# Performance work log

Measured on AMD Instinct MI355X. Metric: run time of the kernel, lower is better.

## Reference

```python
import jax, jax.numpy as jnp
import numpy as np

NUM_GROUPS = 32
EPS = 1e-5


def group_norm(x, w, b):
    # x: [B,C,H,W], 32 groups
    B, C, H, W = x.shape
    xg = x.reshape(B, NUM_GROUPS, C // NUM_GROUPS, H, W)
    mean = xg.mean(axis=(2, 3, 4), keepdims=True)
    var = xg.var(axis=(2, 3, 4), keepdims=True)
    xn = ((xg - mean) * jax.lax.rsqrt(var + EPS)).reshape(B, C, H, W)
    return xn * w[None, :, None, None] + b[None, :, None, None]


def conv1x1(x, w, b):
    # x: [B,C,H,W], w: [O,C], b: [O]
    return jnp.einsum('bchw,oc->bohw', x, w) + b[None, :, None, None]


def setup_inputs() -> dict:
    key = jax.random.key(0)
    ks = jax.random.split(key, 7)
    B, C, H, W = 16, 512, 32, 32
    x = jax.random.normal(ks[0], (B, C, H, W), dtype=jnp.float32)
    gn_w = jnp.ones((C,), dtype=jnp.float32)
    gn_b = jnp.zeros((C,), dtype=jnp.float32)
    s = 1.0 / np.sqrt(C)
    qkv_w = jax.random.normal(ks[1], (3 * C, C), dtype=jnp.float32) * s
    qkv_b = jnp.zeros((3 * C,), dtype=jnp.float32)
    proj_w = jax.random.normal(ks[2], (C, C), dtype=jnp.float32) * s
    proj_b = jnp.zeros((C,), dtype=jnp.float32)
    return {"x": x, "gn_w": gn_w, "gn_b": gn_b, "qkv_w": qkv_w,
            "qkv_b": qkv_b, "proj_w": proj_w, "proj_b": proj_b}


def reference(x, gn_w, gn_b, qkv_w, qkv_b, proj_w, proj_b):
    B, C, H, W = x.shape
    qkv = conv1x1(group_norm(x, gn_w, gn_b), qkv_w, qkv_b)
    q, k, v = jnp.split(qkv, 3, axis=1)
    scale = (C // 8) ** (-0.5)
    # attn: [B, h, w, H, W]
    attn = jnp.einsum('bchw,bcHW->bhwHW', q * scale, k)
    # NOTE: faithful to original torch code: softmax over the LAST axis only
    attn = jax.nn.softmax(attn, axis=-1)
    out = jnp.einsum('bhwHW,bcHW->bchw', attn, v)
    return x + conv1x1(out, proj_w, proj_b)
```

## Files before the change

kernel.cpp:

```cpp
#include <hip/hip_runtime.h>
#include <hip/hip_bf16.h>

#define B_    16
#define C_    512
#define S_    1024
#define NGRP  32
#define CPG   16

typedef __attribute__((ext_vector_type(8))) short  short8;
typedef __attribute__((ext_vector_type(4))) short  short4v;
typedef __attribute__((ext_vector_type(4))) float  floatx4;

__device__ __forceinline__ unsigned short f2bf(float f) {
    __hip_bfloat16 h = __float2bfloat16(f);
    unsigned short u;
    __builtin_memcpy(&u, &h, 2);
    return u;
}

__global__ __launch_bounds__(256)
void gn_fused_kernel(const float* __restrict__ x, const float* __restrict__ w,
                     const float* __restrict__ bias, __hip_bfloat16* __restrict__ xnT) {
    int bg = blockIdx.x;
    int b = bg >> 5, g = bg & 31;
    const float4* xp = (const float4*)(x + (size_t)bg * (CPG * S_));
    int tid = threadIdx.x;

    float4 vv[16];
    float s = 0.f, ss = 0.f;
#pragma unroll
    for (int r = 0; r < 16; ++r) {
        float4 v = xp[r * 256 + tid];
        vv[r] = v;
        s  += v.x + v.y + v.z + v.w;
        ss += v.x*v.x + v.y*v.y + v.z*v.z + v.w*v.w;
    }
    for (int off = 32; off > 0; off >>= 1) {
        s  += __shfl_down(s, off);
        ss += __shfl_down(ss, off);
    }
    __shared__ float red[2][4];
    __shared__ float msh[2];
    int wid = tid >> 6, lane = tid & 63;
    if (lane == 0) { red[0][wid] = s; red[1][wid] = ss; }
    __syncthreads();
    if (tid == 0) {
        float a = 0.f, c = 0.f;
        for (int i = 0; i < 4; ++i) { a += red[0][i]; c += red[1][i]; }
        float mean = a / (float)(CPG * S_);
        float var  = c / (float)(CPG * S_) - mean * mean;
        msh[0] = mean;
        msh[1] = rsqrtf(var + 1e-5f);
    }
    __syncthreads();
    float mean = msh[0], inv = msh[1];

    float sc[16], sh[16];
#pragma unroll
    for (int c = 0; c < 16; ++c) {
        float wc = w[g * 16 + c];
        sc[c] = inv * wc;
        sh[c] = bias[g * 16 + c] - mean * inv * wc;
    }

#pragma unroll
    for (int kk = 0; kk < 4; ++kk) {
        unsigned short outp[16];
#pragma unroll
        for (int c = 0; c < 16; ++c) {
            float v = (kk == 0) ? vv[c].x : (kk == 1) ? vv[c].y : (kk == 2) ? vv[c].z : vv[c].w;
            outp[c] = f2bf(v * sc[c] + sh[c]);
        }
        int srow = 4 * tid + kk;
        unsigned short* dst = (unsigned short*)xnT + ((size_t)(b * S_ + srow) * C_ + g * 16);
        *(short8*)dst       = *(short8*)outp;
        *(short8*)(dst + 8) = *(short8*)(outp + 8);
    }
}

__global__ __launch_bounds__(256)
void prep_kernel(const float* __restrict__ qkv_w, const float* __restrict__ proj_w,
                 const float* __restrict__ qkv_b,
                 unsigned short* __restrict__ bufX,
                 unsigned short* __restrict__ bufY,
                 float* __restrict__ bqWk, float* __restrict__ biasvp)
{
    int blk = blockIdx.x;
    int tid = threadIdx.x;
    if (blk < 192) {
        __shared__ float T[64][65];
        int mat = blk >> 6, tile = blk & 63;
        int r0 = (tile >> 3) * 64, c0 = (tile & 7) * 64;
        const float* src; unsigned short* dst;
        if (mat == 0)      { src = qkv_w + 512 * 512;  dst = bufX; }
        else if (mat == 1) { src = qkv_w;              dst = bufY; }
        else               { src = qkv_w + 1024 * 512; dst = bufY + 262144; }
#pragma unroll
        for (int rr = 0; rr < 4; ++rr) {
            int sr = rr * 16 + (tid >> 4);
            int sc = (tid & 15) * 4;
            float4 v = *(const float4*)(src + (size_t)(c0 + sr) * 512 + r0 + sc);
            T[sc][sr] = v.x; T[sc + 1][sr] = v.y; T[sc + 2][sr] = v.z; T[sc + 3][sr] = v.w;
        }
        __syncthreads();
#pragma unroll
        for (int rr = 0; rr < 4; ++rr) {
            int dr = rr * 16 + (tid >> 4);
            int dc = (tid & 15) * 4;
            short4v o;
            o[0] = (short)f2bf(T[dr][dc]);     o[1] = (short)f2bf(T[dr][dc + 1]);
            o[2] = (short)f2bf(T[dr][dc + 2]); o[3] = (short)f2bf(T[dr][dc + 3]);
            *(short4v*)(dst + (size_t)(r0 + dr) * 512 + c0 + dc) = o;
        }
    } else if (blk < 256) {
        unsigned short* wp = bufX + 262144;
#pragma unroll
        for (int t = 0; t < 4; ++t) {
            int i = (blk - 192) * 4096 + t * 1024 + tid * 4;
            float4 v = *(const float4*)(proj_w + i);
            short4v o;
            o[0] = (short)f2bf(v.x); o[1] = (short)f2bf(v.y);
            o[2] = (short)f2bf(v.z); o[3] = (short)f2bf(v.w);
            *(short4v*)(wp + i) = o;
        }
    } else if (blk < 264) {
        int sub = blk - 256;
        int j = (sub & 1) * 256 + tid;
        int o0 = (sub >> 1) * 128;
        float acc = 0.f;
#pragma unroll 8
        for (int oo = 0; oo < 128; ++oo) {
            int o = o0 + oo;
            acc += qkv_b[o] * qkv_w[(size_t)(512 + o) * 512 + j];
        }
        atomicAdd(&bqWk[j], acc);
    } else {
        int wv = tid >> 6, lane = tid & 63;
        int c = (blk - 264) * 4 + wv;
        float s = 0.f;
#pragma unroll
        for (int t = 0; t < 8; ++t)
            s += proj_w[(size_t)c * 512 + t * 64 + lane] * qkv_b[1024 + t * 64 + lane];
        for (int off = 32; off > 0; off >>= 1) s += __shfl_down(s, off);
        if (lane == 0) biasvp[c] = s;
    }
}

template<int BIAS_MODE, bool OUT_BF16, bool RESID, bool SWIZ, int KTOT>
__global__ __launch_bounds__(256)
void mfma_gemm(const unsigned short* __restrict__ A, const unsigned short* __restrict__ Bm,
               const float* __restrict__ bias, const float* __restrict__ resid,
               void* __restrict__ Yv,
               int lda, int ldb, int ldy,
               size_t sA, size_t sB, size_t sY, size_t sR, float alpha,
               int ntsh, int nxsh)
{
    __shared__ unsigned short As[2 * 128 * 32];
    __shared__ unsigned short Bs[2 * 128 * 32];
    int bx, by, bz;
    if (SWIZ) {
        int lin = blockIdx.x;
        int xcd = lin & 7, sup = lin >> 3;
        bz = xcd + ((sup >> ntsh) << 3);
        int tile = sup & ((1 << ntsh) - 1);
        bx = tile & ((1 << nxsh) - 1);
        by = tile >> nxsh;
    } else { bx = blockIdx.x; by = blockIdx.y; bz = blockIdx.z; }

    const unsigned short* Ab = A  + (size_t)bz * sA;
    const unsigned short* Bb = Bm + (size_t)bz * sB;
    const int tid = threadIdx.x, wave = tid >> 6, lane = tid & 63;
    const int m0 = by * 128, n0 = bx * 128;
    const int wr = wave >> 1, wc = wave & 1, lr = lane & 15, kq = lane >> 4;
    const int row0 = tid >> 2, kc0 = (tid & 3) << 3;

    floatx4 acc[4][4] = {};

    for (int k0 = 0; k0 < KTOT; k0 += 64) {
        __syncthreads();
#pragma unroll
        for (int kk = 0; kk < 2; ++kk) {
#pragma unroll
            for (int r = 0; r < 2; ++r) {
                const unsigned short* ga = Ab + (size_t)(m0 + r * 64 + row0) * lda + k0 + kk * 32 + kc0;
                __builtin_amdgcn_global_load_lds(
                    (const __attribute__((address_space(1))) void*)ga,
                    (__attribute__((address_space(3))) void*)(As + kk * 4096 + (r * 256 + wave * 64) * 8),
                    16, 0, 0);
                const unsigned short* gb = Bb + (size_t)(n0 + r * 64 + row0) * ldb + k0 + kk * 32 + kc0;
                __builtin_amdgcn_global_load_lds(
                    (const __attribute__((address_space(1))) void*)gb,
                    (__attribute__((address_space(3))) void*)(Bs + kk * 4096 + (r * 256 + wave * 64) * 8),
                    16, 0, 0);
            }
        }
        __syncthreads();

#pragma unroll
        for (int kk = 0; kk < 2; ++kk) {
            short8 af[4], bfr[4];
#pragma unroll
            for (int i = 0; i < 4; ++i)
                af[i] = *(const short8*)&As[kk * 4096 + (wr * 64 + i * 16 + lr) * 32 + kq * 8];
#pragma unroll
            for (int j = 0; j < 4; ++j)
                bfr[j] = *(const short8*)&Bs[kk * 4096 + (wc * 64 + j * 16 + lr) * 32 + kq * 8];
#pragma unroll
            for (int i = 0; i < 4; ++i)
#pragma unroll
                for (int j = 0; j < 4; ++j)
                    acc[i][j] = __builtin_amdgcn_mfma_f32_16x16x32_bf16(af[i], bfr[j], acc[i][j], 0, 0, 0);
        }
    }

    const size_t ybase = (size_t)bz * sY;
    const size_t rbase = (size_t)bz * sR;
#pragma unroll
    for (int i = 0; i < 4; ++i) {
#pragma unroll
        for (int r = 0; r < 4; ++r) {
            int m = m0 + wr * 64 + i * 16 + kq * 4 + r;
            float bm = (BIAS_MODE == 1) ? bias[m] : 0.f;
#pragma unroll
            for (int j = 0; j < 4; ++j) {
                int n = n0 + wc * 64 + j * 16 + lr;
                float vv = acc[i][j][r] * alpha + bm;
                if (BIAS_MODE == 2) vv += bias[n];
                if (RESID) vv += resid[rbase + (size_t)m * ldy + n];
                if (OUT_BF16)
                    ((__hip_bfloat16*)Yv)[ybase + (size_t)m * ldy + n] = __float2bfloat16(vv);
                else
                    ((float*)Yv)[ybase + (size_t)m * ldy + n] = vv;
            }
        }
    }
}

__global__ __launch_bounds__(512)
void scores_softmax8(const unsigned short* __restrict__ A,
                     const unsigned short* __restrict__ Bm,
                     unsigned short* __restrict__ P)
{
    __shared__ __align__(16) unsigned short lds[65536];
    char* asb = (char*)lds;
    char* bsb = (char*)lds + 65536;

    const int bid = blockIdx.x;
    const int bz = bid >> 4, t16 = bid & 15;
    const int by = t16 >> 2, bx = t16 & 3;
    const int m0 = by << 8, n0 = bx << 8;

    const size_t sAB = (size_t)S_ * 512;
    const unsigned short* Ab = A  + (size_t)bz * sAB;
    const unsigned short* Bb = Bm + (size_t)bz * sAB;

    const int tid = threadIdx.x, wave = tid >> 6, lane = tid & 63;
    const int wr = wave >> 2, wc = wave & 3;
    const int lr = lane & 15, kq = lane >> 4;
    const int swz = (lr & 7) << 4;

    floatx4 acc[8][4] = {};
    short8 aF[4][2], bF[2][2][2];

    auto stage = [&](const unsigned short* __restrict__ G, int row0, int t,
                     char* base, int buf, int half) {
#pragma unroll
        for (int c = 0; c < 2; ++c) {
            int x = c * 8192 + tid * 16;
            int row = x >> 7;
            int colb = (x & 127) ^ ((row & 7) << 4);
            const unsigned short* ga = G + (((size_t)(row0 + row)) << 9) + (t << 6) + (colb >> 1);
            char* ldst = base + buf * 32768 + half * 16384 + c * 8192 + wave * 1024;
            __builtin_amdgcn_global_load_lds(
                (const __attribute__((address_space(1))) void*)ga,
                (__attribute__((address_space(3))) void*)ldst, 16, 0, 0);
        }
    };
    auto rdA = [&](int buf, int mh, int ii, int kk) {
        int byte = buf * 32768 + wr * 16384 + (mh * 64 + ii * 16 + lr) * 128
                 + ((kk * 64 + kq * 16) ^ swz);
        return *(const short8*)(asb + byte);
    };
    auto rdB = [&](int buf, int nh, int jj, int kk) {
        int trow = wc * 64 + (nh * 2 + jj) * 16 + lr;
        int byte = buf * 32768 + (trow >> 7) * 16384 + (trow & 127) * 128
                 + ((kk * 64 + kq * 16) ^ swz);
        return *(const short8*)(bsb + byte);
    };

    stage(Ab, m0,       0, asb, 0, 0);
    stage(Bb, n0,       0, bsb, 0, 0);
    stage(Bb, n0 + 128, 0, bsb, 0, 1);
    stage(Ab, m0 + 128, 0, asb, 0, 1);
    stage(Ab, m0,       1, asb, 1, 0);
    stage(Bb, n0,       1, bsb, 1, 0);
    stage(Bb, n0 + 128, 1, bsb, 1, 1);
    asm volatile("s_waitcnt vmcnt(6)" ::: "memory");
    __builtin_amdgcn_s_barrier();

    for (int t = 0; t < 8; ++t) {
        const int buf = t & 1;
#pragma unroll
        for (int ii = 0; ii < 4; ++ii) { aF[ii][0] = rdA(buf, 0, ii, 0); aF[ii][1] = rdA(buf, 0, ii, 1); }
#pragma unroll
        for (int jj = 0; jj < 2; ++jj) { bF[0][jj][0] = rdB(buf, 0, jj, 0); bF[0][jj][1] = rdB(buf, 0, jj, 1); }
        if (t < 7) stage(Ab, m0 + 128, t + 1, asb, (t + 1) & 1, 1);
        __builtin_amdgcn_s_barrier();
        asm volatile("s_waitcnt lgkmcnt(0)" ::: "memory");
        __builtin_amdgcn_s_setprio(1);
#pragma unroll
        for (int ii = 0; ii < 4; ++ii)
#pragma unroll
            for (int jj = 0; jj < 2; ++jj)
#pragma unroll
                for (int kk = 0; kk < 2; ++kk)
                    acc[ii][jj] = __builtin_amdgcn_mfma_f32_16x16x32_bf16(aF[ii][kk], bF[0][jj][kk], acc[ii][jj], 0, 0, 0);
        __builtin_amdgcn_s_setprio(0);
        __builtin_amdgcn_s_barrier();
#pragma unroll
        for (int jj = 0; jj < 2; ++jj) { bF[1][jj][0] = rdB(buf, 1, jj, 0); bF[1][jj][1] = rdB(buf, 1, jj, 1); }
        __builtin_amdgcn_s_barrier();
        asm volatile("s_waitcnt lgkmcnt(0)" ::: "memory");
        __builtin_amdgcn_s_setprio(1);
#pragma unroll
        for (int ii = 0; ii < 4; ++ii)
#pragma unroll
            for (int jj = 0; jj < 2; ++jj)
#pragma unroll
                for (int kk = 0; kk < 2; ++kk)
                    acc[ii][2 + jj] = __builtin_amdgcn_mfma_f32_16x16x32_bf16(aF[ii][kk], bF[1][jj][kk], acc[ii][2 + jj], 0, 0, 0);
        __builtin_amdgcn_s_setprio(0);
        __builtin_amdgcn_s_barrier();
#pragma unroll
        for (int ii = 0; ii < 4; ++ii) { aF[ii][0] = rdA(buf, 1, ii, 0); aF[ii][1] = rdA(buf, 1, ii, 1); }
        if (t < 6) stage(Bb, n0, t + 2, bsb, buf, 0);
        __builtin_amdgcn_s_barrier();
        asm volatile("s_waitcnt lgkmcnt(0)" ::: "memory");
        __builtin_amdgcn_s_setprio(1);
#pragma unroll
        for (int ii = 0; ii < 4; ++ii)
#pragma unroll
            for (int jj = 0; jj < 2; ++jj)
#pragma unroll
                for (int kk = 0; kk < 2; ++kk)
                    acc[4 + ii][2 + jj] = __builtin_amdgcn_mfma_f32_16x16x32_bf16(aF[ii][kk], bF[1][jj][kk], acc[4 + ii][2 + jj], 0, 0, 0);
        __builtin_amdgcn_s_setprio(0);
        __builtin_amdgcn_s_barrier();
        if (t < 6) {
            stage(Ab, m0,       t + 2, asb, buf, 0);
            stage(Bb, n0 + 128, t + 2, bsb, buf, 1);
        }
        __builtin_amdgcn_s_setprio(1);
#pragma unroll
        for (int ii = 0; ii < 4; ++ii)
#pragma unroll
            for (int jj = 0; jj < 2; ++jj)
#pragma unroll
                for (int kk = 0; kk < 2; ++kk)
                    acc[4 + ii][jj] = __builtin_amdgcn_mfma_f32_16x16x32_bf16(aF[ii][kk], bF[0][jj][kk], acc[4 + ii][jj], 0, 0, 0);
        __builtin_amdgcn_s_setprio(0);
        if (t < 6) { asm volatile("s_waitcnt vmcnt(6)" ::: "memory"); }
        else       { asm volatile("s_waitcnt vmcnt(0)" ::: "memory"); }
        __builtin_amdgcn_s_barrier();
    }

#pragma unroll
    for (int j = 0; j < 4; ++j) {
        int sqc = wc * 64 + j * 16 + lr;
        int srow = sqc * 512;
        int sxor = (sqc & 7) << 4;
#pragma unroll
        for (int h = 0; h < 4; ++h) {
            float v0[4], v1[4];
            float mx = -1e30f;
#pragma unroll
            for (int r = 0; r < 4; ++r) {
                v0[r] = acc[2 * h][j][r]     * 0.125f;
                v1[r] = acc[2 * h + 1][j][r] * 0.125f;
                mx = fmaxf(mx, fmaxf(v0[r], v1[r]));
            }
            mx = fmaxf(mx, __shfl_xor(mx, 16));
            mx = fmaxf(mx, __shfl_xor(mx, 32));
            float sm = 0.f;
#pragma unroll
            for (int r = 0; r < 4; ++r) {
                v0[r] = __expf(v0[r] - mx);
                v1[r] = __expf(v1[r] - mx);
                sm += v0[r] + v1[r];
            }
            sm += __shfl_xor(sm, 16);
            sm += __shfl_xor(sm, 32);
            float inv = 1.f / sm;
            short4v p0, p1;
#pragma unroll
            for (int r = 0; r < 4; ++r) {
                p0[r] = (short)f2bf(v0[r] * inv);
                p1[r] = (short)f2bf(v1[r] * inv);
            }
            int kb = (wr * 128 + h * 32 + kq * 4) * 2;
            *(short4v*)(asb + ((srow + kb) ^ sxor))      = p0;
            *(short4v*)(asb + ((srow + kb + 32) ^ sxor)) = p1;
        }
    }
    __syncthreads();

    const size_t pbase = ((size_t)bz << 20) + (size_t)n0 * 1024 + m0;
#pragma unroll
    for (int it = 0; it < 16; ++it) {
        int row = wave * 32 + it * 2 + (lane >> 5);
        int colb = (lane & 31) << 4;
        short8 v = *(const short8*)(asb + ((row * 512 + colb) ^ ((row & 7) << 4)));
        *(short8*)(P + pbase + (size_t)row * 1024 + (colb >> 1)) = v;
    }
}

extern "C" void kernel_launch(void* const* d_in, const int* in_sizes, int n_in,
                              void* d_out, int out_size, void* d_ws, size_t ws_size,
                              hipStream_t stream) {
    const float* x     = (const float*)d_in[0];
    const float* gn_w  = (const float*)d_in[1];
    const float* gn_b  = (const float*)d_in[2];
    const float* qkv_w = (const float*)d_in[3];
    const float* qkv_b = (const float*)d_in[4];
    const float* pr_w  = (const float*)d_in[5];
    const float* pr_b  = (const float*)d_in[6];
    float* out = (float*)d_out;

    char* w = (char*)d_ws;
    __hip_bfloat16* xnT  = (__hip_bfloat16*)w;
    __hip_bfloat16* u    = (__hip_bfloat16*)(w + (16u << 20));
    __hip_bfloat16* Vp   = (__hip_bfloat16*)(w + (32u << 20));
    __hip_bfloat16* P    = (__hip_bfloat16*)(w + (48u << 20));
    unsigned short* bufX = (unsigned short*)(w + (80u << 20));
    unsigned short* bufY = (unsigned short*)(w + (81u << 20));
    unsigned short* bufZ = (unsigned short*)(w + (82u << 20));
    float*          bqWk = (float*)(w + (83u << 20));
    float*          bvp  = (float*)(w + (83u << 20) + 4096);

    hipMemsetAsync(bqWk, 0, 512 * sizeof(float), stream);

    prep_kernel<<<392, 256, 0, stream>>>(qkv_w, pr_w, qkv_b, bufX, bufY, bqWk, bvp);

    gn_fused_kernel<<<B_ * NGRP, 256, 0, stream>>>(x, gn_w, gn_b, xnT);

    mfma_gemm<0, true, false, false, 512><<<dim3(4, 4, 2), 256, 0, stream>>>(
        bufX, bufY, nullptr, nullptr, bufZ,
        512, 512, 512, 262144, 262144, 262144, 0, 1.f, 0, 0);

    mfma_gemm<2, true, false, false, 512><<<dim3(4, 128, 1), 256, 0, stream>>>(
        (const unsigned short*)xnT, bufZ, bqWk, nullptr, u,
        512, 512, 512, 0, 0, 0, 0, 1.f, 0, 0);

    mfma_gemm<1, true, false, true, 512><<<512, 256, 0, stream>>>(
        bufZ + 262144, (const unsigned short*)xnT, bvp, nullptr, Vp,
        512, 512, 1024, 0, (size_t)S_ * 512, (size_t)512 * S_, 0, 1.f, 5, 3);

    scores_softmax8<<<256, 512, 0, stream>>>(
        (const unsigned short*)xnT, (const unsigned short*)u, (unsigned short*)P);

    mfma_gemm<1, false, true, true, 1024><<<512, 256, 0, stream>>>(
        (const unsigned short*)Vp, (const unsigned short*)P, pr_b, x, out,
        1024, 1024, 1024, (size_t)512 * S_, (size_t)S_ * S_, (size_t)512 * S_,
        (size_t)512 * S_, 1.f, 5, 3);
}
```

Baseline: 209.6 us.

## Replace three GEMMs with 8-wave 128x256 tile kernel using phased LDS pipeline

Adds a new 512-thread GEMM kernel with 128x256 tiles that loads via global_load_lds into an XOR-swizzled double buffer. The inner loop is split into four MFMA phases, with barriers and s_setprio interleaving the LDS reads and next-tile loads with compute. The Q-proj, V-proj and final output GEMMs switch to it, with grid and swizzle shifts adjusted for the larger tiles. The goal is better latency hiding and data reuse per block. In exchange it uses more LDS per block, lowers occupancy and halves the block count.

```diff
diff --git a/kernel.cpp b/kernel.cpp
--- a/kernel.cpp
+++ b/kernel.cpp
@@ -236,6 +236,161 @@
     }
 }
 
+template<int BIAS_MODE, bool OUT_BF16, bool RESID, bool SWIZ, int KTOT>
+__global__ __launch_bounds__(512)
+void gemm8ph(const unsigned short* __restrict__ A, const unsigned short* __restrict__ Bm,
+             const float* __restrict__ bias, const float* __restrict__ resid,
+             void* __restrict__ Yv,
+             int lda, int ldb, int ldy,
+             size_t sA, size_t sB, size_t sY, size_t sR, float alpha,
+             int ntsh, int nxsh)
+{
+    __shared__ __align__(16) char lds[98304];
+    char* asb = lds;
+    char* bsb = lds + 32768;
+
+    int bx, by, bz;
+    if (SWIZ) {
+        int lin = blockIdx.x;
+        int xcd = lin & 7, sup = lin >> 3;
+        bz = xcd + ((sup >> ntsh) << 3);
+        int tile = sup & ((1 << ntsh) - 1);
+        bx = tile & ((1 << nxsh) - 1);
+        by = tile >> nxsh;
+    } else { bx = blockIdx.x; by = blockIdx.y; bz = blockIdx.z; }
+
+    const unsigned short* Ab = A  + (size_t)bz * sA;
+    const unsigned short* Bb = Bm + (size_t)bz * sB;
+    const int tid = threadIdx.x, wave = tid >> 6, lane = tid & 63;
+    const int m0 = by * 128, n0 = bx * 256;
+    const int wr = wave >> 2, wc = wave & 3;
+    const int lr = lane & 15, kq = lane >> 4;
+    const int swz = (lr & 7) << 4;
+
+    floatx4 acc[4][4] = {};
+    short8 aF[2][2], bF[2][2][2];
+
+    auto stage = [&](const unsigned short* __restrict__ G, int ld, int grow,
+                     int t, char* dstbase) {
+#pragma unroll
+        for (int c = 0; c < 2; ++c) {
+            int x = c * 8192 + tid * 16;
+            int row = x >> 7;
+            int colb = (x & 127) ^ ((row & 7) << 4);
+            const unsigned short* ga = G + (size_t)(grow + row) * ld + t * 64 + (colb >> 1);
+            char* ldst = dstbase + c * 8192 + wave * 1024;
+            __builtin_amdgcn_global_load_lds(
+                (const __attribute__((address_space(1))) void*)ga,
+                (__attribute__((address_space(3))) void*)ldst, 16, 0, 0);
+        }
+    };
+    auto rdA = [&](int buf, int i, int kk) {
+        int byte = buf * 16384 + (wr * 64 + i * 16 + lr) * 128
+                 + ((kk * 64 + kq * 16) ^ swz);
+        return *(const short8*)(asb + byte);
+    };
+    auto rdB = [&](int buf, int jn, int kk) {
+        int row = wc * 64 + jn * 16 + lr;
+        int byte = buf * 32768 + (row >> 7) * 16384 + (row & 127) * 128
+                 + ((kk * 64 + kq * 16) ^ swz);
+        return *(const short8*)(bsb + byte);
+    };
+
+    stage(Ab, lda, m0,       0, asb);
+    stage(Bb, ldb, n0,       0, bsb);
+    stage(Bb, ldb, n0 + 128, 0, bsb + 16384);
+    stage(Bb, ldb, n0,       1, bsb + 32768);
+    stage(Bb, ldb, n0 + 128, 1, bsb + 32768 + 16384);
+    asm volatile("s_waitcnt vmcnt(4)" ::: "memory");
+    __builtin_amdgcn_s_barrier();
+
+    constexpr int NT = KTOT / 64;
+    for (int t = 0; t < NT; ++t) {
+        const int buf = t & 1;
+#pragma unroll
+        for (int ii = 0; ii < 2; ++ii) { aF[ii][0] = rdA(buf, ii, 0); aF[ii][1] = rdA(buf, ii, 1); }
+#pragma unroll
+        for (int jj = 0; jj < 2; ++jj) { bF[0][jj][0] = rdB(buf, jj, 0); bF[0][jj][1] = rdB(buf, jj, 1); }
+        if (t < NT - 1) stage(Ab, lda, m0, t + 1, asb + ((t + 1) & 1) * 16384);
+        __builtin_amdgcn_s_barrier();
+        asm volatile("s_waitcnt lgkmcnt(0)" ::: "memory");
+        __builtin_amdgcn_s_setprio(1);
+#pragma unroll
+        for (int ii = 0; ii < 2; ++ii)
+#pragma unroll
+            for (int jj = 0; jj < 2; ++jj)
+#pragma unroll
+                for (int kk = 0; kk < 2; ++kk)
+                    acc[ii][jj] = __builtin_amdgcn_mfma_f32_16x16x32_bf16(aF[ii][kk], bF[0][jj][kk], acc[ii][jj], 0, 0, 0);
+        __builtin_amdgcn_s_setprio(0);
+        __builtin_amdgcn_s_barrier();
+#pragma unroll
+        for (int jj = 0; jj < 2; ++jj) { bF[1][jj][0] = rdB(buf, 2 + jj, 0); bF[1][jj][1] = rdB(buf, 2 + jj, 1); }
+        __builtin_amdgcn_s_barrier();
+        asm volatile("s_waitcnt lgkmcnt(0)" ::: "memory");
+        __builtin_amdgcn_s_setprio(1);
+#pragma unroll
+        for (int ii = 0; ii < 2; ++ii)
+#pragma unroll
+            for (int jj = 0; jj < 2; ++jj)
+#pragma unroll
+                for (int kk = 0; kk < 2; ++kk)
+                    acc[ii][2 + jj] = __builtin_amdgcn_mfma_f32_16x16x32_bf16(aF[ii][kk], bF[1][jj][kk], acc[ii][2 + jj], 0, 0, 0);
+        __builtin_amdgcn_s_setprio(0);
+        __builtin_amdgcn_s_barrier();
+#pragma unroll
+        for (int ii = 0; ii < 2; ++ii) { aF[ii][0] = rdA(buf, 2 + ii, 0); aF[ii][1] = rdA(buf, 2 + ii, 1); }
+        if (t < NT - 2) stage(Bb, ldb, n0, t + 2, bsb + buf * 32768);
+        __builtin_amdgcn_s_barrier();
+        asm volatile("s_waitcnt lgkmcnt(0)" ::: "memory");
+        __builtin_amdgcn_s_setprio(1);
+#pragma unroll
+        for (int ii = 0; ii < 2; ++ii)
+#pragma unroll
+            for (int jj = 0; jj < 2; ++jj)
+#pragma unroll
+                for (int kk = 0; kk < 2; ++kk)
+                    acc[2 + ii][2 + jj] = __builtin_amdgcn_mfma_f32_16x16x32_bf16(aF[ii][kk], bF[1][jj][kk], acc[2 + ii][2 + jj], 0, 0, 0);
+        __builtin_amdgcn_s_setprio(0);
+        __builtin_amdgcn_s_barrier();
+        if (t < NT - 2) stage(Bb, ldb, n0 + 128, t + 2, bsb + buf * 32768 + 16384);
+        __builtin_amdgcn_s_setprio(1);
+#pragma unroll
+        for (int ii = 0; ii < 2; ++ii)
+#pragma unroll
+            for (int jj = 0; jj < 2; ++jj)
+#pragma unroll
+                for (int kk = 0; kk < 2; ++kk)
+                    acc[2 + ii][jj] = __builtin_amdgcn_mfma_f32_16x16x32_bf16(aF[ii][kk], bF[0][jj][kk], acc[2 + ii][jj], 0, 0, 0);
+        __builtin_amdgcn_s_setprio(0);
+        if (t < NT - 2) { asm volatile("s_waitcnt vmcnt(4)" ::: "memory"); }
+        else            { asm volatile("s_waitcnt vmcnt(0)" ::: "memory"); }
+        __builtin_amdgcn_s_barrier();
+    }
+
+    const size_t ybase = (size_t)bz * sY;
+    const size_t rbase = (size_t)bz * sR;
+#pragma unroll
+    for (int i = 0; i < 4; ++i) {
+#pragma unroll
+        for (int r = 0; r < 4; ++r) {
+            int m = m0 + wr * 64 + i * 16 + kq * 4 + r;
+            float bm = (BIAS_MODE == 1) ? bias[m] : 0.f;
+#pragma unroll
+            for (int j = 0; j < 4; ++j) {
+                int n = n0 + wc * 64 + j * 16 + lr;
+                float vv = acc[i][j][r] * alpha + bm;
+                if (BIAS_MODE == 2) vv += bias[n];
+                if (RESID) vv += resid[rbase + (size_t)m * ldy + n];
+                if (OUT_BF16)
+                    ((__hip_bfloat16*)Yv)[ybase + (size_t)m * ldy + n] = __float2bfloat16(vv);
+                else
+                    ((float*)Yv)[ybase + (size_t)m * ldy + n] = vv;
+            }
+        }
+    }
+}
+
 __global__ __launch_bounds__(512)
 void scores_softmax8(const unsigned short* __restrict__ A,
                      const unsigned short* __restrict__ Bm,
@@ -447,19 +602,19 @@
         bufX, bufY, nullptr, nullptr, bufZ,
         512, 512, 512, 262144, 262144, 262144, 0, 1.f, 0, 0);
 
-    mfma_gemm<2, true, false, false, 512><<<dim3(4, 128, 1), 256, 0, stream>>>(
+    gemm8ph<2, true, false, false, 512><<<dim3(2, 128, 1), 512, 0, stream>>>(
         (const unsigned short*)xnT, bufZ, bqWk, nullptr, u,
         512, 512, 512, 0, 0, 0, 0, 1.f, 0, 0);
 
-    mfma_gemm<1, true, false, true, 512><<<512, 256, 0, stream>>>(
+    gemm8ph<1, true, false, true, 512><<<256, 512, 0, stream>>>(
         bufZ + 262144, (const unsigned short*)xnT, bvp, nullptr, Vp,
-        512, 512, 1024, 0, (size_t)S_ * 512, (size_t)512 * S_, 0, 1.f, 5, 3);
+        512, 512, 1024, 0, (size_t)S_ * 512, (size_t)512 * S_, 0, 1.f, 4, 2);
 
     scores_softmax8<<<256, 512, 0, stream>>>(
         (const unsigned short*)xnT, (const unsigned short*)u, (unsigned short*)P);
 
-    mfma_gemm<1, false, true, true, 1024><<<512, 256, 0, stream>>>(
+    gemm8ph<1, false, true, true, 1024><<<256, 512, 0, stream>>>(
         (const unsigned short*)Vp, (const unsigned short*)P, pr_b, x, out,
         1024, 1024, 1024, (size_t)512 * S_, (size_t)S_ * S_, (size_t)512 * S_,
-        (size_t)512 * S_, 1.f, 5, 3);
+        (size_t)512 * S_, 1.f, 4, 2);
 }
```

Measured after the change: 197.8 us. 1.06x faster.
